# Kernel optimization log

Hardware: AMD Instinct MI355X
Metric: run time of the kernel (lower is better)

## Reference

```python
import jax, jax.numpy as jnp
import numpy as np

P, T, L, K, N, K2, M, D = 16384, 8, 4096, 16, 2048, 32, 8, 64
ITER = 8
MM = {'flow_traffic': (0.0, 1e-4), 'flow_packets': (0.0, 1e-3), 'flow_packet_size': (0.0, 1e-3), 'link_capacity': (0.0, 1e-2)}


def _mlp2(x, w1, b1, w2, b2):
    return jax.nn.relu(jax.nn.relu(x @ w1 + b1) @ w2 + b2)


def _gru(x_proj, h, wh, bh):
    # Keras GRUCell, reset_after=True, gate order (z, r, h)
    hp = h @ wh + bh
    xz, xr, xc = jnp.split(x_proj, 3, axis=-1)
    hz, hr, hc = jnp.split(hp, 3, axis=-1)
    z = jax.nn.sigmoid(xz + hz)
    r = jax.nn.sigmoid(xr + hr)
    c = jnp.tanh(xc + r * hc)
    return z * h + (1.0 - z) * c


def setup_inputs() -> dict:
    key = jax.random.key(0)
    ks = iter(jax.random.split(key, 64))
    f32, i32 = jnp.float32, jnp.int32
    rn = lambda shape: jax.random.normal(next(ks), shape, dtype=f32) * 0.05
    inp = {}
    inp['flow_traffic'] = jax.random.uniform(next(ks), (P, 1), f32, 1.0, 1000.0)
    inp['flow_packets'] = jax.random.uniform(next(ks), (P, 1), f32, 1.0, 100.0)
    inp['flow_packet_size'] = jax.random.uniform(next(ks), (P, 1), f32, 64.0, 1500.0)
    inp['link_capacity'] = jax.random.uniform(next(ks), (L, 1), f32, 10.0, 100.0)
    inp['pe_w1'] = rn((3, D)); inp['pe_b1'] = jnp.zeros((D,), f32)
    inp['pe_w2'] = rn((D, D)); inp['pe_b2'] = jnp.zeros((D,), f32)
    inp['le_w1'] = rn((3, D)); inp['le_b1'] = jnp.zeros((D,), f32)
    inp['le_w2'] = rn((D, D)); inp['le_b2'] = jnp.zeros((D,), f32)
    inp['de_w1'] = rn((2, D)); inp['de_b1'] = jnp.zeros((D,), f32)
    inp['de_w2'] = rn((D, D)); inp['de_b2'] = jnp.zeros((D,), f32)
    for p in ('pgru', 'lgru', 'dgru'):
        inp[p + '_wx'] = rn((D, 3 * D)); inp[p + '_wh'] = rn((D, 3 * D))
        inp[p + '_bx'] = jnp.zeros((3 * D,), f32); inp[p + '_bh'] = jnp.zeros((3 * D,), f32)
    inp['ro_w1'] = rn((D, D // 2)); inp['ro_b1'] = jnp.zeros((D // 2,), f32)
    inp['ro_w2'] = rn((D // 2, D // 4)); inp['ro_b2'] = jnp.zeros((D // 4,), f32)
    inp['ro_w3'] = rn((D // 4, 1)); inp['ro_b3'] = jnp.zeros((1,), f32)
    inp['link_to_path'] = jax.random.randint(next(ks), (P, T), 0, L, i32)
    inp['node_to_path'] = jax.random.randint(next(ks), (P, T), 0, N, i32)
    inp['path_to_link'] = jnp.stack([jax.random.randint(next(ks), (L, K), 0, P, i32),
                                     jax.random.randint(next(ks), (L, K), 1, T + 1, i32)], axis=-1)
    inp['path_to_node'] = jnp.stack([jax.random.randint(next(ks), (N, K2), 0, P, i32),
                                     jax.random.randint(next(ks), (N, K2), 1, T + 1, i32)], axis=-1)
    inp['link_to_node'] = jax.random.randint(next(ks), (N, M), 0, L, i32)
    inp['nodes'] = jnp.zeros((N,), i32)
    inp['link_device_type'] = jnp.zeros((L,), i32)
    return inp


def reference(flow_traffic, flow_packets, flow_packet_size, link_capacity,
              pe_w1, pe_b1, pe_w2, pe_b2, le_w1, le_b1, le_w2, le_b2,
              de_w1, de_b1, de_w2, de_b2,
              pgru_wx, pgru_wh, pgru_bx, pgru_bh,
              lgru_wx, lgru_wh, lgru_bx, lgru_bh,
              dgru_wx, dgru_wh, dgru_bx, dgru_bh,
              ro_w1, ro_b1, ro_w2, ro_b2, ro_w3, ro_b3,
              link_to_path, node_to_path, path_to_link, path_to_node,
              link_to_node, nodes, link_device_type):
    # one_hot depth=1 -> 1.0 iff value==0
    ldt = (link_device_type == 0).astype(jnp.float32)[:, None]  # [L,1]
    # link load from path traffic
    load = flow_traffic[path_to_link[:, :, 0]].sum(axis=1) / (link_capacity * 1e9)  # [L,1]
    path_in = jnp.concatenate([
        (flow_traffic - MM['flow_traffic'][0]) * MM['flow_traffic'][1],
        (flow_packets - MM['flow_packets'][0]) * MM['flow_packets'][1],
        (flow_packet_size - MM['flow_packet_size'][0]) * MM['flow_packet_size'][1]], axis=1)
    path_state = _mlp2(path_in, pe_w1, pe_b1, pe_w2, pe_b2)  # [P,D]
    link_in = jnp.concatenate([(link_capacity - MM['link_capacity'][0]) * MM['link_capacity'][1], load, ldt], axis=1)
    link_state = _mlp2(link_in, le_w1, le_b1, le_w2, le_b2)  # [L,D]
    device_link_mean = link_state[link_to_node].sum(axis=1).mean(axis=1, keepdims=True)  # [N,1]
    devices_encoded = (nodes == 0).astype(jnp.float32)[:, None]  # [N,1]
    device_state = _mlp2(jnp.concatenate([devices_encoded, device_link_mean], axis=1),
                         de_w1, de_b1, de_w2, de_b2)  # [N,D]
    pl0, pl1 = path_to_link[:, :, 0], path_to_link[:, :, 1]
    pn0, pn1 = path_to_node[:, :, 0], path_to_node[:, :, 1]
    pss = None
    for _ in range(ITER):
        x = link_state[link_to_path] + device_state[node_to_path]  # [P,T,D]
        prev = path_state
        x_proj = jnp.swapaxes(x @ pgru_wx + pgru_bx, 0, 1)  # [T,P,3D]

        def step(h, xp):
            h2 = _gru(xp, h, pgru_wh, pgru_bh)
            return h2, h2

        path_state, seq = jax.lax.scan(step, path_state, x_proj)
        pss = jnp.concatenate([prev[:, None], jnp.swapaxes(seq, 0, 1)], axis=1)  # [P,T+1,D]
        link_state = _gru(pss[pl0, pl1].sum(axis=1) @ lgru_wx + lgru_bx, link_state, lgru_wh, lgru_bh)
        device_state = _gru(pss[pn0, pn1].sum(axis=1) @ dgru_wx + dgru_bx, device_state, dgru_wh, dgru_bh)
    h = jax.nn.relu(pss[:, 1:] @ ro_w1 + ro_b1)
    h = jax.nn.relu(h @ ro_w2 + ro_b2)
    occupancy = jax.nn.softplus(h @ ro_w3 + ro_b3)  # [P,T,1]
    delay = (occupancy / link_capacity[link_to_path]).sum(axis=1)  # [P,1]
    return delay
```

## Files before the change

kernel.cpp:

```cpp
#include <hip/hip_runtime.h>
#include <hip/hip_bf16.h>

static constexpr int PN = 16384;
static constexpr int TT = 8;
static constexpr int LN = 4096;
static constexpr int KG = 16;
static constexpr int NN = 2048;
static constexpr int K2G = 32;
static constexpr int MG = 8;
static constexpr int ITER = 8;

typedef __attribute__((ext_vector_type(8))) short short8b;
typedef __attribute__((ext_vector_type(4))) float f32x4;
typedef __attribute__((ext_vector_type(4))) unsigned int u32x4;

__device__ __forceinline__ float frcp(float x) {
    return __builtin_amdgcn_rcpf(x);
}
__device__ __forceinline__ float sigmoidf_(float x) {
    return frcp(1.0f + __expf(-x));
}
__device__ __forceinline__ float tanhf_(float x) {
    return 1.0f - 2.0f * frcp(__expf(2.0f * x) + 1.0f);
}
__device__ __forceinline__ float softplusf_(float x) {
    return fmaxf(x, 0.0f) + log1pf(__expf(-fabsf(x)));
}
__device__ __forceinline__ unsigned short f2bf(float f) {
    unsigned int x = __float_as_uint(f);
    unsigned int r = (x + 0x7fffu + ((x >> 16) & 1u)) >> 16;
    return (unsigned short)r;
}
__device__ __forceinline__ unsigned int pk2bf(float a, float b) {
    union { __hip_bfloat162 h; unsigned int u; } cvt;
    cvt.h = __float22bfloat162_rn(float2{a, b});
    return cvt.u;
}
__device__ __forceinline__ float bf2f(unsigned short u) {
    return __uint_as_float(((unsigned int)u) << 16);
}

__global__ __launch_bounds__(256) void k_setup(
    const float* __restrict__ ft, const float* __restrict__ fpk,
    const float* __restrict__ fps, const float* __restrict__ cap,
    const int* __restrict__ ptl, const int* __restrict__ ldt,
    const float* __restrict__ pe_w1, const float* __restrict__ pe_b1,
    const float* __restrict__ pe_w2, const float* __restrict__ pe_b2,
    const float* __restrict__ le_w1, const float* __restrict__ le_b1,
    const float* __restrict__ le_w2, const float* __restrict__ le_b2,
    const float* __restrict__ pgru_wx, const float* __restrict__ pgru_wh,
    const float* __restrict__ lgru_wx, const float* __restrict__ lgru_wh,
    const float* __restrict__ dgru_wx, const float* __restrict__ dgru_wh,
    unsigned short* __restrict__ pwxT, unsigned short* __restrict__ pwhT,
    unsigned short* __restrict__ lwxT, unsigned short* __restrict__ lwhT,
    unsigned short* __restrict__ dwxT, unsigned short* __restrict__ dwhT,
    float* __restrict__ path_state, float* __restrict__ link_state)
{
    int b = blockIdx.x;
    int tid = threadIdx.x;
    if (b >= 1280) {
        const float* srcs[6] = {pgru_wx, pgru_wh, lgru_wx, lgru_wh, dgru_wx, dgru_wh};
        unsigned short* dsts[6] = {pwxT, pwhT, lwxT, lwhT, dwxT, dwhT};
        int i = (b - 1280) * 256 + tid;
        int mi = i / 12288, o = i - mi * 12288;
        int n = o >> 6, k = o & 63;
        dsts[mi][o] = f2bf(srcs[mi][k * 192 + n]);
        return;
    }
    __shared__ __align__(16) float w2s[4096];
    __shared__ float w1s[192], b1s[64], b2s[64];
    __shared__ float h1s[4][64];
    bool isPath = (b < 1024);
    const float* w1p = isPath ? pe_w1 : le_w1;
    const float* b1p = isPath ? pe_b1 : le_b1;
    const float* w2p = isPath ? pe_w2 : le_w2;
    const float* b2p = isPath ? pe_b2 : le_b2;
    for (int i = tid; i < 4096; i += 256) w2s[i] = w2p[i];
    if (tid < 192) w1s[tid] = w1p[tid];
    if (tid < 64) { b1s[tid] = b1p[tid]; b2s[tid] = b2p[tid]; }
    __syncthreads();
    int rl = tid >> 6, d = tid & 63;
    int base = (isPath ? b : (b - 1024)) * 16;
    for (int rp = 0; rp < 4; ++rp) {
        int row = base + rp * 4 + rl;
        float h;
        if (isPath) {
            float x0 = ft[row]  * 1e-4f;
            float x1 = fpk[row] * 1e-3f;
            float x2 = fps[row] * 1e-3f;
            h = b1s[d] + x0 * w1s[d] + x1 * w1s[64 + d] + x2 * w1s[128 + d];
        } else {
            float v = 0.0f;
            if (d < 16) v = ft[ptl[(row * 16 + d) * 2]];
            v += __shfl_down(v, 8);
            v += __shfl_down(v, 4);
            v += __shfl_down(v, 2);
            v += __shfl_down(v, 1);
            float ssum = __shfl(v, 0);
            float cv = cap[row];
            float load = ssum * frcp(cv * 1e9f);
            float x2 = (ldt[row] == 0) ? 1.0f : 0.0f;
            h = b1s[d] + cv * 0.01f * w1s[d] + load * w1s[64 + d] + x2 * w1s[128 + d];
        }
        h1s[rl][d] = fmaxf(h, 0.0f);
        __syncthreads();
        float acc = b2s[d];
#pragma unroll 8
        for (int k = 0; k < 64; ++k) acc += h1s[rl][k] * w2s[k * 64 + d];
        float* dst = isPath ? path_state : link_state;
        dst[(size_t)row * 64 + d] = fmaxf(acc, 0.0f);
        __syncthreads();
    }
}

__global__ __launch_bounds__(256) void k_device_encode(
    const float* __restrict__ link_state, const int* __restrict__ ltn,
    const int* __restrict__ nodes,
    const float* __restrict__ w1, const float* __restrict__ b1,
    const float* __restrict__ w2, const float* __restrict__ b2,
    float* __restrict__ device_state)
{
    __shared__ __align__(16) float w2s[4096];
    __shared__ float h1s[4][64];
    int tid = threadIdx.x;
    for (int i = tid; i < 4096; i += 256) w2s[i] = w2[i];
    int rl = tid >> 6, d = tid & 63;
    int row = blockIdx.x * 4 + rl;
    float s = 0.0f;
#pragma unroll
    for (int m = 0; m < MG; ++m)
        s += link_state[(size_t)ltn[row * MG + m] * 64 + d];
#pragma unroll
    for (int o = 32; o > 0; o >>= 1) s += __shfl_xor(s, o);
    float dlm = s * (1.0f / 64.0f);
    float enc = (nodes[row] == 0) ? 1.0f : 0.0f;
    float h = b1[d] + enc * w1[d] + dlm * w1[64 + d];
    h1s[rl][d] = fmaxf(h, 0.0f);
    __syncthreads();
    float acc = b2[d];
#pragma unroll 8
    for (int k = 0; k < 64; ++k) acc += h1s[rl][k] * w2s[k * 64 + d];
    device_state[(size_t)row * 64 + d] = fmaxf(acc, 0.0f);
}

template <bool LAST>
__global__ __launch_bounds__(256, 4) void k_pscan(
    const float* __restrict__ ls, const float* __restrict__ dst,
    const int* __restrict__ ltp, const int* __restrict__ ntp,
    const unsigned short* __restrict__ wxT,
    const unsigned short* __restrict__ whT,
    const float* __restrict__ bx, const float* __restrict__ bh,
    float* __restrict__ path_state, unsigned short* __restrict__ pssb,
    const float* __restrict__ rw1, const float* __restrict__ rb1,
    const float* __restrict__ rw2, const float* __restrict__ rb2,
    const float* __restrict__ rw3, const float* __restrict__ rb3,
    const float* __restrict__ cap, float* __restrict__ out)
{
    __shared__ __align__(16) unsigned short Xs[8][16][72];
    __shared__ __align__(16) unsigned short Hb0[16][72];
    __shared__ int sIdx[256];
    __shared__ __align__(16) float rw1s[LAST ? 2048 : 4];
    __shared__ __align__(16) float rw2s[LAST ? 512 : 4];
    __shared__ float rw3s[16], rb1s[32], rb2s[16];
    int tid = threadIdx.x;
    int p0 = blockIdx.x * 16;

    if (LAST) {
        for (int i = tid; i < 2048; i += 256) rw1s[i] = rw1[i];
        for (int i = tid; i < 512; i += 256) rw2s[i] = rw2[i];
        if (tid < 16) rw3s[tid] = rw3[tid];
        if (tid < 32) rb1s[tid] = rb1[tid];
        if (tid < 16) rb2s[tid] = rb2[tid];
    }
    {
        int pi = tid >> 1;
        int m = pi & 15, t = pi >> 4;
        int gi = (p0 + m) * TT + t;
        sIdx[tid] = (tid & 1) ? __builtin_nontemporal_load(ntp + gi)
                              : __builtin_nontemporal_load(ltp + gi);
    }
    __syncthreads();
    {
        int j = tid & 15;
        int g = tid >> 4;
#pragma unroll
        for (int ro = 0; ro < 8; ++ro) {
            int pi = ro * 16 + g;
            int il = sIdx[pi * 2];
            int in = sIdx[pi * 2 + 1];
            float4 a = *(const float4*)(ls + (size_t)il * 64 + j * 4);
            float4 b = *(const float4*)(dst + (size_t)in * 64 + j * 4);
            uint2 u;
            u.x = pk2bf(a.x + b.x, a.y + b.y);
            u.y = pk2bf(a.z + b.z, a.w + b.w);
            *(uint2*)&Xs[ro][g][j * 4] = u;
        }
    }

    int lane = tid & 63, w = tid >> 6;
    int c = lane & 15, q = lane >> 4;
    int d = 16 * w + c;
    short8b fx[3][2], fh[3][2];
#pragma unroll
    for (int g = 0; g < 3; ++g)
#pragma unroll
        for (int kt = 0; kt < 2; ++kt) {
            int off = (g * 64 + 16 * w + c) * 64 + kt * 32 + q * 8;
            fx[g][kt] = *(const short8b*)(wxT + off);
            fh[g][kt] = *(const short8b*)(whT + off);
        }
    float bz = bx[d] + bh[d];
    float br = bx[64 + d] + bh[64 + d];
    float bxc = bx[128 + d];
    float bhc = bh[128 + d];
    float hold[4];
#pragma unroll
    for (int r_ = 0; r_ < 4; ++r_) {
        hold[r_] = path_state[(size_t)(p0 + q * 4 + r_) * 64 + d];
        Hb0[q * 4 + r_][d] = f2bf(hold[r_]);
    }
    __syncthreads();

    short8b aXc0 = *(const short8b*)&Xs[0][c][q * 8];
    short8b aXc1 = *(const short8b*)&Xs[0][c][32 + q * 8];

    for (int t = 0; t < TT; ++t) {
        f32x4 ax[3], ah[3];
        ax[0] = (f32x4){bz, bz, bz, bz};
        ax[1] = (f32x4){br, br, br, br};
        ax[2] = (f32x4){bxc, bxc, bxc, bxc};
        ah[0] = (f32x4){0.f, 0.f, 0.f, 0.f};
        ah[1] = (f32x4){0.f, 0.f, 0.f, 0.f};
        ah[2] = (f32x4){bhc, bhc, bhc, bhc};
        const unsigned short* hsrc = (t == 0) ? &Hb0[0][0] : &Xs[t - 1][0][0];
        short8b aH0 = *(const short8b*)(hsrc + c * 72 + q * 8);
        short8b aH1 = *(const short8b*)(hsrc + c * 72 + 32 + q * 8);
#pragma unroll
        for (int g = 0; g < 3; ++g) {
            ax[g] = __builtin_amdgcn_mfma_f32_16x16x32_bf16(aXc0, fx[g][0], ax[g], 0, 0, 0);
            ax[g] = __builtin_amdgcn_mfma_f32_16x16x32_bf16(aXc1, fx[g][1], ax[g], 0, 0, 0);
            ah[g] = __builtin_amdgcn_mfma_f32_16x16x32_bf16(aH0, fh[g][0], ah[g], 0, 0, 0);
            ah[g] = __builtin_amdgcn_mfma_f32_16x16x32_bf16(aH1, fh[g][1], ah[g], 0, 0, 0);
        }
        if (t < TT - 1) {
            aXc0 = *(const short8b*)&Xs[t + 1][c][q * 8];
            aXc1 = *(const short8b*)&Xs[t + 1][c][32 + q * 8];
        }
#pragma unroll
        for (int r_ = 0; r_ < 4; ++r_) {
            float z  = sigmoidf_(ax[0][r_] + ah[0][r_]);
            float rr = sigmoidf_(ax[1][r_] + ah[1][r_]);
            float cc = tanhf_(ax[2][r_] + rr * ah[2][r_]);
            float hn = cc + z * (hold[r_] - cc);
            hold[r_] = hn;
            Xs[t][q * 4 + r_][d] = f2bf(hn);
        }
        __syncthreads();
    }
    if (!LAST) {
#pragma unroll
        for (int r_ = 0; r_ < 4; ++r_)
            path_state[(size_t)(p0 + q * 4 + r_) * 64 + d] = hold[r_];
        {
            unsigned short* base = pssb + (size_t)p0 * TT * 64;
#pragma unroll
            for (int j = 0; j < 4; ++j) {
                int o = j * 2048 + tid * 8;
                int r = o >> 6;
                int c0 = o & 63;
                int m = r >> 3, t = r & 7;
                u32x4 v = *(const u32x4*)&Xs[t][m][c0];
                __builtin_nontemporal_store(v, (u32x4*)(base + o));
            }
        }
        return;
    }
    {
        int r = tid >> 1, hh = tid & 1;
        int m = r >> 3, t = r & 7;
        short8b rowv[8];
#pragma unroll
        for (int j = 0; j < 8; ++j)
            rowv[j] = *(const short8b*)&Xs[t][m][j * 8];
        float a1[16];
#pragma unroll
        for (int i = 0; i < 16; ++i) a1[i] = 0.f;
#pragma unroll 4
        for (int k = 0; k < 64; ++k) {
            float x = bf2f((unsigned short)rowv[k >> 3][k & 7]);
            const float* wr = &rw1s[k * 32 + hh * 16];
            float4 wa = *(const float4*)(wr);
            float4 wb = *(const float4*)(wr + 4);
            float4 wc = *(const float4*)(wr + 8);
            float4 wd = *(const float4*)(wr + 12);
            a1[0]  += x * wa.x; a1[1]  += x * wa.y; a1[2]  += x * wa.z; a1[3]  += x * wa.w;
            a1[4]  += x * wb.x; a1[5]  += x * wb.y; a1[6]  += x * wb.z; a1[7]  += x * wb.w;
            a1[8]  += x * wc.x; a1[9]  += x * wc.y; a1[10] += x * wc.z; a1[11] += x * wc.w;
            a1[12] += x * wd.x; a1[13] += x * wd.y; a1[14] += x * wd.z; a1[15] += x * wd.w;
        }
#pragma unroll
        for (int i = 0; i < 16; ++i)
            a1[i] = fmaxf(a1[i] + rb1s[hh * 16 + i], 0.0f);
        float h1[32];
#pragma unroll
        for (int i = 0; i < 16; ++i) {
            float o = __shfl_xor(a1[i], 1);
            h1[hh * 16 + i] = a1[i];
            h1[(1 - hh) * 16 + i] = o;
        }
        float a2[8];
#pragma unroll
        for (int i = 0; i < 8; ++i) a2[i] = 0.f;
#pragma unroll 4
        for (int k = 0; k < 32; ++k) {
            float x = h1[k];
            const float* wr = &rw2s[k * 16 + hh * 8];
            float4 wa = *(const float4*)(wr);
            float4 wb = *(const float4*)(wr + 4);
            a2[0] += x * wa.x; a2[1] += x * wa.y; a2[2] += x * wa.z; a2[3] += x * wa.w;
            a2[4] += x * wb.x; a2[5] += x * wb.y; a2[6] += x * wb.z; a2[7] += x * wb.w;
        }
#pragma unroll
        for (int i = 0; i < 8; ++i)
            a2[i] = fmaxf(a2[i] + rb2s[hh * 8 + i], 0.0f);
        float h2[16];
#pragma unroll
        for (int i = 0; i < 8; ++i) {
            float o = __shfl_xor(a2[i], 1);
            h2[hh * 8 + i] = a2[i];
            h2[(1 - hh) * 8 + i] = o;
        }
        float a3 = rb3[0];
#pragma unroll
        for (int k = 0; k < 16; ++k) a3 += h2[k] * rw3s[k];
        float occ = softplusf_(a3);
        float dcon = occ * frcp(cap[ltp[(p0 + m) * TT + t]]);
        float s = dcon;
        s += __shfl_xor(s, 2);
        s += __shfl_xor(s, 4);
        s += __shfl_xor(s, 8);
        if ((tid & 15) == 0) out[p0 + m] = s;
    }
}

template <int Kg>
__device__ __forceinline__ void edge_body(
    const unsigned short* __restrict__ wxT, const unsigned short* __restrict__ whT,
    const float* __restrict__ bx, const float* __restrict__ bh,
    const int* __restrict__ p2e, const unsigned short* __restrict__ pssb,
    float* __restrict__ state, int blk)
{
    __shared__ int idxs[16 * Kg * 2];
    __shared__ __align__(16) unsigned short Ab[16][72];
    __shared__ __align__(16) unsigned short Hbs[16][72];
    __shared__ __align__(16) float Hf[16][68];
    int tid = threadIdx.x;
    int r0 = blk * 16;
    for (int i = tid; i < 16 * Kg * 2; i += 256)
        idxs[i] = p2e[(size_t)r0 * Kg * 2 + i];
    __syncthreads();
    {
        int r = tid >> 4, c4 = (tid & 15) * 4;
        int row = r0 + r;
        float4 s = {0.f, 0.f, 0.f, 0.f};
#pragma unroll
        for (int k = 0; k < Kg; ++k) {
            int pi = idxs[(r * Kg + k) * 2];
            int ti = idxs[(r * Kg + k) * 2 + 1];
            ushort4 v = *(const ushort4*)(pssb + ((size_t)pi * TT + ti - 1) * 64 + c4);
            s.x += bf2f(v.x); s.y += bf2f(v.y);
            s.z += bf2f(v.z); s.w += bf2f(v.w);
        }
        uint2 ua;
        ua.x = pk2bf(s.x, s.y); ua.y = pk2bf(s.z, s.w);
        *(uint2*)&Ab[r][c4] = ua;
        float4 hv = *(const float4*)(state + (size_t)row * 64 + c4);
        *(float4*)&Hf[r][c4] = hv;
        uint2 uh;
        uh.x = pk2bf(hv.x, hv.y); uh.y = pk2bf(hv.z, hv.w);
        *(uint2*)&Hbs[r][c4] = uh;
    }
    __syncthreads();
    int lane = tid & 63, w = tid >> 6;
    int c = lane & 15, q = lane >> 4;
    int d = 16 * w + c;
    short8b fx[3][2], fh[3][2];
#pragma unroll
    for (int g = 0; g < 3; ++g)
#pragma unroll
        for (int kt = 0; kt < 2; ++kt) {
            int off = (g * 64 + 16 * w + c) * 64 + kt * 32 + q * 8;
            fx[g][kt] = *(const short8b*)(wxT + off);
            fh[g][kt] = *(const short8b*)(whT + off);
        }
    float bz = bx[d] + bh[d];
    float br = bx[64 + d] + bh[64 + d];
    float bxc = bx[128 + d];
    float bhc = bh[128 + d];
    f32x4 ax[3], ah[3];
    ax[0] = (f32x4){bz, bz, bz, bz};
    ax[1] = (f32x4){br, br, br, br};
    ax[2] = (f32x4){bxc, bxc, bxc, bxc};
    ah[0] = (f32x4){0.f, 0.f, 0.f, 0.f};
    ah[1] = (f32x4){0.f, 0.f, 0.f, 0.f};
    ah[2] = (f32x4){bhc, bhc, bhc, bhc};
#pragma unroll
    for (int kt = 0; kt < 2; ++kt) {
        short8b aA = *(const short8b*)&Ab[c][kt * 32 + q * 8];
        short8b aH = *(const short8b*)&Hbs[c][kt * 32 + q * 8];
#pragma unroll
        for (int g = 0; g < 3; ++g) {
            ax[g] = __builtin_amdgcn_mfma_f32_16x16x32_bf16(aA, fx[g][kt], ax[g], 0, 0, 0);
            ah[g] = __builtin_amdgcn_mfma_f32_16x16x32_bf16(aH, fh[g][kt], ah[g], 0, 0, 0);
        }
    }
#pragma unroll
    for (int r = 0; r < 4; ++r) {
        int m = q * 4 + r;
        float z  = sigmoidf_(ax[0][r] + ah[0][r]);
        float rr = sigmoidf_(ax[1][r] + ah[1][r]);
        float cc = tanhf_(ax[2][r] + rr * ah[2][r]);
        float hn = cc + z * (Hf[m][d] - cc);
        state[(size_t)(r0 + m) * 64 + d] = hn;
    }
}

__global__ __launch_bounds__(256) void k_edge_merged(
    const unsigned short* __restrict__ lwxT, const unsigned short* __restrict__ lwhT,
    const float* __restrict__ lbx, const float* __restrict__ lbh,
    const int* __restrict__ ptl,
    const unsigned short* __restrict__ dwxT, const unsigned short* __restrict__ dwhT,
    const float* __restrict__ dbx, const float* __restrict__ dbh,
    const int* __restrict__ ptn,
    const unsigned short* __restrict__ pssb,
    float* __restrict__ link_state, float* __restrict__ device_state)
{
    int b = blockIdx.x;
    if (b < LN / 16) {
        edge_body<KG>(lwxT, lwhT, lbx, lbh, ptl, pssb, link_state, b);
    } else {
        edge_body<K2G>(dwxT, dwhT, dbx, dbh, ptn, pssb, device_state, b - LN / 16);
    }
}

extern "C" void kernel_launch(void* const* d_in, const int* in_sizes, int n_in,
                              void* d_out, int out_size, void* d_ws, size_t ws_size,
                              hipStream_t stream) {
    const float* ft   = (const float*)d_in[0];
    const float* fpk  = (const float*)d_in[1];
    const float* fps  = (const float*)d_in[2];
    const float* cap  = (const float*)d_in[3];
    const float* pe_w1 = (const float*)d_in[4];
    const float* pe_b1 = (const float*)d_in[5];
    const float* pe_w2 = (const float*)d_in[6];
    const float* pe_b2 = (const float*)d_in[7];
    const float* le_w1 = (const float*)d_in[8];
    const float* le_b1 = (const float*)d_in[9];
    const float* le_w2 = (const float*)d_in[10];
    const float* le_b2 = (const float*)d_in[11];
    const float* de_w1 = (const float*)d_in[12];
    const float* de_b1 = (const float*)d_in[13];
    const float* de_w2 = (const float*)d_in[14];
    const float* de_b2 = (const float*)d_in[15];
    const float* pgru_wx = (const float*)d_in[16];
    const float* pgru_wh = (const float*)d_in[17];
    const float* pgru_bx = (const float*)d_in[18];
    const float* pgru_bh = (const float*)d_in[19];
    const float* lgru_wx = (const float*)d_in[20];
    const float* lgru_wh = (const float*)d_in[21];
    const float* lgru_bx = (const float*)d_in[22];
    const float* lgru_bh = (const float*)d_in[23];
    const float* dgru_wx = (const float*)d_in[24];
    const float* dgru_wh = (const float*)d_in[25];
    const float* dgru_bx = (const float*)d_in[26];
    const float* dgru_bh = (const float*)d_in[27];
    const float* ro_w1 = (const float*)d_in[28];
    const float* ro_b1 = (const float*)d_in[29];
    const float* ro_w2 = (const float*)d_in[30];
    const float* ro_b2 = (const float*)d_in[31];
    const float* ro_w3 = (const float*)d_in[32];
    const float* ro_b3 = (const float*)d_in[33];
    const int* ltp   = (const int*)d_in[34];
    const int* ntp   = (const int*)d_in[35];
    const int* ptl   = (const int*)d_in[36];
    const int* ptn   = (const int*)d_in[37];
    const int* ltn   = (const int*)d_in[38];
    const int* nodes = (const int*)d_in[39];
    const int* ldt   = (const int*)d_in[40];
    float* out = (float*)d_out;

    char* ws = (char*)d_ws;
    float* path_state = (float*)ws;      ws += (size_t)PN * 64 * 4;
    float* link_state = (float*)ws;      ws += (size_t)LN * 64 * 4;
    float* device_state = (float*)ws;    ws += (size_t)NN * 64 * 4;
    unsigned short* pssb = (unsigned short*)ws; ws += (size_t)PN * TT * 64 * 2;
    unsigned short* pwxT = (unsigned short*)ws; ws += 192 * 64 * 2;
    unsigned short* pwhT = (unsigned short*)ws; ws += 192 * 64 * 2;
    unsigned short* lwxT = (unsigned short*)ws; ws += 192 * 64 * 2;
    unsigned short* lwhT = (unsigned short*)ws; ws += 192 * 64 * 2;
    unsigned short* dwxT = (unsigned short*)ws; ws += 192 * 64 * 2;
    unsigned short* dwhT = (unsigned short*)ws; ws += 192 * 64 * 2;

    k_setup<<<1568, 256, 0, stream>>>(ft, fpk, fps, cap, ptl, ldt,
                                      pe_w1, pe_b1, pe_w2, pe_b2,
                                      le_w1, le_b1, le_w2, le_b2,
                                      pgru_wx, pgru_wh, lgru_wx, lgru_wh,
                                      dgru_wx, dgru_wh,
                                      pwxT, pwhT, lwxT, lwhT, dwxT, dwhT,
                                      path_state, link_state);
    k_device_encode<<<NN / 4, 256, 0, stream>>>(link_state, ltn, nodes, de_w1,
                                                de_b1, de_w2, de_b2, device_state);
    for (int it = 0; it < ITER - 1; ++it) {
        k_pscan<false><<<PN / 16, 256, 0, stream>>>(
            link_state, device_state, ltp, ntp, pwxT, pwhT, pgru_bx, pgru_bh,
            path_state, pssb, ro_w1, ro_b1, ro_w2, ro_b2, ro_w3, ro_b3, cap, out);
        k_edge_merged<<<LN / 16 + NN / 16, 256, 0, stream>>>(
            lwxT, lwhT, lgru_bx, lgru_bh, ptl,
            dwxT, dwhT, dgru_bx, dgru_bh, ptn,
            pssb, link_state, device_state);
    }
    k_pscan<true><<<PN / 16, 256, 0, stream>>>(
        link_state, device_state, ltp, ntp, pwxT, pwhT, pgru_bx, pgru_bh,
        path_state, pssb, ro_w1, ro_b1, ro_w2, ro_b2, ro_w3, ro_b3, cap, out);
}
```

Before: 388.3 us.

## Make each wave own 16 paths in k_pscan to drop block barriers

Restructures the path GRU scan so each wavefront independently processes 16 paths across all 64 output columns, with per-wave shared-memory slices. The block grows to 64 paths and the per-timestep __syncthreads disappear, since each wave only reads its own LDS region. It removes barrier stalls in the serial 8-step recurrence. In exchange each wave holds all 48 weight fragments in registers and launch bounds drop to 1, which raises register pressure and may lower occupancy. There are also 4x fewer blocks.

```diff
diff --git a/kernel.cpp b/kernel.cpp
--- a/kernel.cpp
+++ b/kernel.cpp
@@ -144,7 +144,7 @@
 }
 
 template <bool LAST>
-__global__ __launch_bounds__(256, 4) void k_pscan(
+__global__ __launch_bounds__(256, 1) void k_pscan(
     const float* __restrict__ ls, const float* __restrict__ dst,
     const int* __restrict__ ltp, const int* __restrict__ ntp,
     const unsigned short* __restrict__ wxT,
@@ -156,14 +156,16 @@
     const float* __restrict__ rw3, const float* __restrict__ rb3,
     const float* __restrict__ cap, float* __restrict__ out)
 {
-    __shared__ __align__(16) unsigned short Xs[8][16][72];
-    __shared__ __align__(16) unsigned short Hb0[16][72];
-    __shared__ int sIdx[256];
+    __shared__ __align__(16) unsigned short Xs[4][8][16][72];
+    __shared__ __align__(16) unsigned short Hb0[4][16][72];
+    __shared__ int sIdx[4][256];
     __shared__ __align__(16) float rw1s[LAST ? 2048 : 4];
     __shared__ __align__(16) float rw2s[LAST ? 512 : 4];
     __shared__ float rw3s[16], rb1s[32], rb2s[16];
     int tid = threadIdx.x;
-    int p0 = blockIdx.x * 16;
+    int wi = tid >> 6, lane = tid & 63;
+    int c = lane & 15, q = lane >> 4;
+    int p0w = blockIdx.x * 64 + wi * 16;
 
     if (LAST) {
         for (int i = tid; i < 2048; i += 256) rw1s[i] = rw1[i];
@@ -172,174 +174,201 @@
         if (tid < 32) rb1s[tid] = rb1[tid];
         if (tid < 16) rb2s[tid] = rb2[tid];
     }
-    {
-        int pi = tid >> 1;
+
+    unsigned short (*XsW)[16][72] = Xs[wi];
+    unsigned short (*Hb0W)[72] = Hb0[wi];
+    int* sIdxW = sIdx[wi];
+
+#pragma unroll
+    for (int k = 0; k < 4; ++k) {
+        int i = k * 64 + lane;
+        int pi = i >> 1;
         int m = pi & 15, t = pi >> 4;
-        int gi = (p0 + m) * TT + t;
-        sIdx[tid] = (tid & 1) ? __builtin_nontemporal_load(ntp + gi)
-                              : __builtin_nontemporal_load(ltp + gi);
-    }
-    __syncthreads();
-    {
-        int j = tid & 15;
-        int g = tid >> 4;
-#pragma unroll
-        for (int ro = 0; ro < 8; ++ro) {
-            int pi = ro * 16 + g;
-            int il = sIdx[pi * 2];
-            int in = sIdx[pi * 2 + 1];
-            float4 a = *(const float4*)(ls + (size_t)il * 64 + j * 4);
-            float4 b = *(const float4*)(dst + (size_t)in * 64 + j * 4);
-            uint2 u;
-            u.x = pk2bf(a.x + b.x, a.y + b.y);
-            u.y = pk2bf(a.z + b.z, a.w + b.w);
-            *(uint2*)&Xs[ro][g][j * 4] = u;
-        }
-    }
-
-    int lane = tid & 63, w = tid >> 6;
-    int c = lane & 15, q = lane >> 4;
-    int d = 16 * w + c;
-    short8b fx[3][2], fh[3][2];
+        int gi = (p0w + m) * TT + t;
+        sIdxW[i] = (i & 1) ? __builtin_nontemporal_load(ntp + gi)
+                           : __builtin_nontemporal_load(ltp + gi);
+    }
+
+    short8b fx[3][4][2], fh[3][4][2];
 #pragma unroll
     for (int g = 0; g < 3; ++g)
 #pragma unroll
-        for (int kt = 0; kt < 2; ++kt) {
-            int off = (g * 64 + 16 * w + c) * 64 + kt * 32 + q * 8;
-            fx[g][kt] = *(const short8b*)(wxT + off);
-            fh[g][kt] = *(const short8b*)(whT + off);
-        }
-    float bz = bx[d] + bh[d];
-    float br = bx[64 + d] + bh[64 + d];
-    float bxc = bx[128 + d];
-    float bhc = bh[128 + d];
-    float hold[4];
-#pragma unroll
-    for (int r_ = 0; r_ < 4; ++r_) {
-        hold[r_] = path_state[(size_t)(p0 + q * 4 + r_) * 64 + d];
-        Hb0[q * 4 + r_][d] = f2bf(hold[r_]);
-    }
-    __syncthreads();
-
-    short8b aXc0 = *(const short8b*)&Xs[0][c][q * 8];
-    short8b aXc1 = *(const short8b*)&Xs[0][c][32 + q * 8];
-
+        for (int ct = 0; ct < 4; ++ct)
+#pragma unroll
+            for (int kt = 0; kt < 2; ++kt) {
+                int off = (g * 64 + ct * 16 + c) * 64 + kt * 32 + q * 8;
+                fx[g][ct][kt] = *(const short8b*)(wxT + off);
+                fh[g][ct][kt] = *(const short8b*)(whT + off);
+            }
+    float bzv[4], brv[4], bxcv[4], bhcv[4];
+#pragma unroll
+    for (int ct = 0; ct < 4; ++ct) {
+        int dd = ct * 16 + c;
+        bzv[ct]  = bx[dd] + bh[dd];
+        brv[ct]  = bx[64 + dd] + bh[64 + dd];
+        bxcv[ct] = bx[128 + dd];
+        bhcv[ct] = bh[128 + dd];
+    }
+
+#pragma unroll
+    for (int ro = 0; ro < 32; ++ro) {
+        int pi = ro * 4 + q;
+        int t = pi >> 4, m = pi & 15;
+        int il = sIdxW[pi * 2];
+        int in = sIdxW[pi * 2 + 1];
+        float4 a = *(const float4*)(ls + (size_t)il * 64 + c * 4);
+        float4 b = *(const float4*)(dst + (size_t)in * 64 + c * 4);
+        uint2 u;
+        u.x = pk2bf(a.x + b.x, a.y + b.y);
+        u.y = pk2bf(a.z + b.z, a.w + b.w);
+        *(uint2*)&XsW[t][m][c * 4] = u;
+    }
+
+    float hold[4][4];
+#pragma unroll
+    for (int r_ = 0; r_ < 4; ++r_)
+#pragma unroll
+        for (int ct = 0; ct < 4; ++ct) {
+            hold[ct][r_] = path_state[(size_t)(p0w + q * 4 + r_) * 64 + ct * 16 + c];
+            Hb0W[q * 4 + r_][ct * 16 + c] = f2bf(hold[ct][r_]);
+        }
+
+    short8b aXc0 = *(const short8b*)&XsW[0][c][q * 8];
+    short8b aXc1 = *(const short8b*)&XsW[0][c][32 + q * 8];
+#pragma unroll
     for (int t = 0; t < TT; ++t) {
-        f32x4 ax[3], ah[3];
-        ax[0] = (f32x4){bz, bz, bz, bz};
-        ax[1] = (f32x4){br, br, br, br};
-        ax[2] = (f32x4){bxc, bxc, bxc, bxc};
-        ah[0] = (f32x4){0.f, 0.f, 0.f, 0.f};
-        ah[1] = (f32x4){0.f, 0.f, 0.f, 0.f};
-        ah[2] = (f32x4){bhc, bhc, bhc, bhc};
-        const unsigned short* hsrc = (t == 0) ? &Hb0[0][0] : &Xs[t - 1][0][0];
+        const unsigned short* hsrc = (t == 0) ? &Hb0W[0][0] : &XsW[t - 1][0][0];
         short8b aH0 = *(const short8b*)(hsrc + c * 72 + q * 8);
         short8b aH1 = *(const short8b*)(hsrc + c * 72 + 32 + q * 8);
-#pragma unroll
-        for (int g = 0; g < 3; ++g) {
-            ax[g] = __builtin_amdgcn_mfma_f32_16x16x32_bf16(aXc0, fx[g][0], ax[g], 0, 0, 0);
-            ax[g] = __builtin_amdgcn_mfma_f32_16x16x32_bf16(aXc1, fx[g][1], ax[g], 0, 0, 0);
-            ah[g] = __builtin_amdgcn_mfma_f32_16x16x32_bf16(aH0, fh[g][0], ah[g], 0, 0, 0);
-            ah[g] = __builtin_amdgcn_mfma_f32_16x16x32_bf16(aH1, fh[g][1], ah[g], 0, 0, 0);
-        }
+        short8b nX0 = aXc0, nX1 = aXc1;
         if (t < TT - 1) {
-            aXc0 = *(const short8b*)&Xs[t + 1][c][q * 8];
-            aXc1 = *(const short8b*)&Xs[t + 1][c][32 + q * 8];
-        }
-#pragma unroll
-        for (int r_ = 0; r_ < 4; ++r_) {
-            float z  = sigmoidf_(ax[0][r_] + ah[0][r_]);
-            float rr = sigmoidf_(ax[1][r_] + ah[1][r_]);
-            float cc = tanhf_(ax[2][r_] + rr * ah[2][r_]);
-            float hn = cc + z * (hold[r_] - cc);
-            hold[r_] = hn;
-            Xs[t][q * 4 + r_][d] = f2bf(hn);
-        }
-        __syncthreads();
-    }
+            nX0 = *(const short8b*)&XsW[t + 1][c][q * 8];
+            nX1 = *(const short8b*)&XsW[t + 1][c][32 + q * 8];
+        }
+#pragma unroll
+        for (int ct = 0; ct < 4; ++ct) {
+            f32x4 ax0 = (f32x4){bzv[ct], bzv[ct], bzv[ct], bzv[ct]};
+            f32x4 ax1 = (f32x4){brv[ct], brv[ct], brv[ct], brv[ct]};
+            f32x4 ax2 = (f32x4){bxcv[ct], bxcv[ct], bxcv[ct], bxcv[ct]};
+            f32x4 ah0 = (f32x4){0.f, 0.f, 0.f, 0.f};
+            f32x4 ah1 = (f32x4){0.f, 0.f, 0.f, 0.f};
+            f32x4 ah2 = (f32x4){bhcv[ct], bhcv[ct], bhcv[ct], bhcv[ct]};
+            ax0 = __builtin_amdgcn_mfma_f32_16x16x32_bf16(aXc0, fx[0][ct][0], ax0, 0, 0, 0);
+            ax0 = __builtin_amdgcn_mfma_f32_16x16x32_bf16(aXc1, fx[0][ct][1], ax0, 0, 0, 0);
+            ax1 = __builtin_amdgcn_mfma_f32_16x16x32_bf16(aXc0, fx[1][ct][0], ax1, 0, 0, 0);
+            ax1 = __builtin_amdgcn_mfma_f32_16x16x32_bf16(aXc1, fx[1][ct][1], ax1, 0, 0, 0);
+            ax2 = __builtin_amdgcn_mfma_f32_16x16x32_bf16(aXc0, fx[2][ct][0], ax2, 0, 0, 0);
+            ax2 = __builtin_amdgcn_mfma_f32_16x16x32_bf16(aXc1, fx[2][ct][1], ax2, 0, 0, 0);
+            ah0 = __builtin_amdgcn_mfma_f32_16x16x32_bf16(aH0, fh[0][ct][0], ah0, 0, 0, 0);
+            ah0 = __builtin_amdgcn_mfma_f32_16x16x32_bf16(aH1, fh[0][ct][1], ah0, 0, 0, 0);
+            ah1 = __builtin_amdgcn_mfma_f32_16x16x32_bf16(aH0, fh[1][ct][0], ah1, 0, 0, 0);
+            ah1 = __builtin_amdgcn_mfma_f32_16x16x32_bf16(aH1, fh[1][ct][1], ah1, 0, 0, 0);
+            ah2 = __builtin_amdgcn_mfma_f32_16x16x32_bf16(aH0, fh[2][ct][0], ah2, 0, 0, 0);
+            ah2 = __builtin_amdgcn_mfma_f32_16x16x32_bf16(aH1, fh[2][ct][1], ah2, 0, 0, 0);
+#pragma unroll
+            for (int r_ = 0; r_ < 4; ++r_) {
+                float z  = sigmoidf_(ax0[r_] + ah0[r_]);
+                float rr = sigmoidf_(ax1[r_] + ah1[r_]);
+                float cc = tanhf_(ax2[r_] + rr * ah2[r_]);
+                float hn = cc + z * (hold[ct][r_] - cc);
+                hold[ct][r_] = hn;
+                XsW[t][q * 4 + r_][ct * 16 + c] = f2bf(hn);
+            }
+        }
+        aXc0 = nX0; aXc1 = nX1;
+    }
+
     if (!LAST) {
 #pragma unroll
         for (int r_ = 0; r_ < 4; ++r_)
-            path_state[(size_t)(p0 + q * 4 + r_) * 64 + d] = hold[r_];
+#pragma unroll
+            for (int ct = 0; ct < 4; ++ct)
+                path_state[(size_t)(p0w + q * 4 + r_) * 64 + ct * 16 + c] = hold[ct][r_];
         {
-            unsigned short* base = pssb + (size_t)p0 * TT * 64;
-#pragma unroll
-            for (int j = 0; j < 4; ++j) {
-                int o = j * 2048 + tid * 8;
+            unsigned short* base = pssb + (size_t)p0w * TT * 64;
+#pragma unroll
+            for (int jj = 0; jj < 8; ++jj) {
+                int o = jj * 512 + lane * 8;
                 int r = o >> 6;
                 int c0 = o & 63;
                 int m = r >> 3, t = r & 7;
-                u32x4 v = *(const u32x4*)&Xs[t][m][c0];
+                u32x4 v = *(const u32x4*)&XsW[t][m][c0];
                 __builtin_nontemporal_store(v, (u32x4*)(base + o));
             }
         }
         return;
     }
+    __syncthreads();
     {
-        int r = tid >> 1, hh = tid & 1;
-        int m = r >> 3, t = r & 7;
-        short8b rowv[8];
-#pragma unroll
-        for (int j = 0; j < 8; ++j)
-            rowv[j] = *(const short8b*)&Xs[t][m][j * 8];
-        float a1[16];
-#pragma unroll
-        for (int i = 0; i < 16; ++i) a1[i] = 0.f;
+        int hh = lane & 1;
+        int rl = lane >> 1;
+#pragma unroll
+        for (int pass = 0; pass < 4; ++pass) {
+            int r = pass * 32 + rl;
+            int m = r >> 3, t = r & 7;
+            short8b rowv[8];
+#pragma unroll
+            for (int j = 0; j < 8; ++j)
+                rowv[j] = *(const short8b*)&XsW[t][m][j * 8];
+            float a1[16];
+#pragma unroll
+            for (int i = 0; i < 16; ++i) a1[i] = 0.f;
 #pragma unroll 4
-        for (int k = 0; k < 64; ++k) {
-            float x = bf2f((unsigned short)rowv[k >> 3][k & 7]);
-            const float* wr = &rw1s[k * 32 + hh * 16];
-            float4 wa = *(const float4*)(wr);
-            float4 wb = *(const float4*)(wr + 4);
-            float4 wc = *(const float4*)(wr + 8);
-            float4 wd = *(const float4*)(wr + 12);
-            a1[0]  += x * wa.x; a1[1]  += x * wa.y; a1[2]  += x * wa.z; a1[3]  += x * wa.w;
-            a1[4]  += x * wb.x; a1[5]  += x * wb.y; a1[6]  += x * wb.z; a1[7]  += x * wb.w;
-            a1[8]  += x * wc.x; a1[9]  += x * wc.y; a1[10] += x * wc.z; a1[11] += x * wc.w;
-            a1[12] += x * wd.x; a1[13] += x * wd.y; a1[14] += x * wd.z; a1[15] += x * wd.w;
-        }
-#pragma unroll
-        for (int i = 0; i < 16; ++i)
-            a1[i] = fmaxf(a1[i] + rb1s[hh * 16 + i], 0.0f);
-        float h1[32];
-#pragma unroll
-        for (int i = 0; i < 16; ++i) {
-            float o = __shfl_xor(a1[i], 1);
-            h1[hh * 16 + i] = a1[i];
-            h1[(1 - hh) * 16 + i] = o;
-        }
-        float a2[8];
-#pragma unroll
-        for (int i = 0; i < 8; ++i) a2[i] = 0.f;
+            for (int k = 0; k < 64; ++k) {
+                float x = bf2f((unsigned short)rowv[k >> 3][k & 7]);
+                const float* wr = &rw1s[k * 32 + hh * 16];
+                float4 wa = *(const float4*)(wr);
+                float4 wb = *(const float4*)(wr + 4);
+                float4 wc = *(const float4*)(wr + 8);
+                float4 wd = *(const float4*)(wr + 12);
+                a1[0]  += x * wa.x; a1[1]  += x * wa.y; a1[2]  += x * wa.z; a1[3]  += x * wa.w;
+                a1[4]  += x * wb.x; a1[5]  += x * wb.y; a1[6]  += x * wb.z; a1[7]  += x * wb.w;
+                a1[8]  += x * wc.x; a1[9]  += x * wc.y; a1[10] += x * wc.z; a1[11] += x * wc.w;
+                a1[12] += x * wd.x; a1[13] += x * wd.y; a1[14] += x * wd.z; a1[15] += x * wd.w;
+            }
+#pragma unroll
+            for (int i = 0; i < 16; ++i)
+                a1[i] = fmaxf(a1[i] + rb1s[hh * 16 + i], 0.0f);
+            float h1[32];
+#pragma unroll
+            for (int i = 0; i < 16; ++i) {
+                float o = __shfl_xor(a1[i], 1);
+                h1[hh * 16 + i] = a1[i];
+                h1[(1 - hh) * 16 + i] = o;
+            }
+            float a2[8];
+#pragma unroll
+            for (int i = 0; i < 8; ++i) a2[i] = 0.f;
 #pragma unroll 4
-        for (int k = 0; k < 32; ++k) {
-            float x = h1[k];
-            const float* wr = &rw2s[k * 16 + hh * 8];
-            float4 wa = *(const float4*)(wr);
-            float4 wb = *(const float4*)(wr + 4);
-            a2[0] += x * wa.x; a2[1] += x * wa.y; a2[2] += x * wa.z; a2[3] += x * wa.w;
-            a2[4] += x * wb.x; a2[5] += x * wb.y; a2[6] += x * wb.z; a2[7] += x * wb.w;
-        }
-#pragma unroll
-        for (int i = 0; i < 8; ++i)
-            a2[i] = fmaxf(a2[i] + rb2s[hh * 8 + i], 0.0f);
-        float h2[16];
-#pragma unroll
-        for (int i = 0; i < 8; ++i) {
-            float o = __shfl_xor(a2[i], 1);
-            h2[hh * 8 + i] = a2[i];
-            h2[(1 - hh) * 8 + i] = o;
-        }
-        float a3 = rb3[0];
-#pragma unroll
-        for (int k = 0; k < 16; ++k) a3 += h2[k] * rw3s[k];
-        float occ = softplusf_(a3);
-        float dcon = occ * frcp(cap[ltp[(p0 + m) * TT + t]]);
-        float s = dcon;
-        s += __shfl_xor(s, 2);
-        s += __shfl_xor(s, 4);
-        s += __shfl_xor(s, 8);
-        if ((tid & 15) == 0) out[p0 + m] = s;
+            for (int k = 0; k < 32; ++k) {
+                float x = h1[k];
+                const float* wr = &rw2s[k * 16 + hh * 8];
+                float4 wa = *(const float4*)(wr);
+                float4 wb = *(const float4*)(wr + 4);
+                a2[0] += x * wa.x; a2[1] += x * wa.y; a2[2] += x * wa.z; a2[3] += x * wa.w;
+                a2[4] += x * wb.x; a2[5] += x * wb.y; a2[6] += x * wb.z; a2[7] += x * wb.w;
+            }
+#pragma unroll
+            for (int i = 0; i < 8; ++i)
+                a2[i] = fmaxf(a2[i] + rb2s[hh * 8 + i], 0.0f);
+            float h2[16];
+#pragma unroll
+            for (int i = 0; i < 8; ++i) {
+                float o = __shfl_xor(a2[i], 1);
+                h2[hh * 8 + i] = a2[i];
+                h2[(1 - hh) * 8 + i] = o;
+            }
+            float a3 = rb3[0];
+#pragma unroll
+            for (int k = 0; k < 16; ++k) a3 += h2[k] * rw3s[k];
+            float occ = softplusf_(a3);
+            float dcon = occ * frcp(cap[sIdxW[(t * 16 + m) * 2]]);
+            float s = dcon;
+            s += __shfl_xor(s, 2);
+            s += __shfl_xor(s, 4);
+            s += __shfl_xor(s, 8);
+            if ((lane & 15) == 0) out[p0w + pass * 4 + (lane >> 4)] = s;
+        }
     }
 }
 
@@ -511,7 +540,7 @@
     k_device_encode<<<NN / 4, 256, 0, stream>>>(link_state, ltn, nodes, de_w1,
                                                 de_b1, de_w2, de_b2, device_state);
     for (int it = 0; it < ITER - 1; ++it) {
-        k_pscan<false><<<PN / 16, 256, 0, stream>>>(
+        k_pscan<false><<<PN / 64, 256, 0, stream>>>(
             link_state, device_state, ltp, ntp, pwxT, pwhT, pgru_bx, pgru_bh,
             path_state, pssb, ro_w1, ro_b1, ro_w2, ro_b2, ro_w3, ro_b3, cap, out);
         k_edge_merged<<<LN / 16 + NN / 16, 256, 0, stream>>>(
@@ -519,7 +548,7 @@
             dwxT, dwhT, dgru_bx, dgru_bh, ptn,
             pssb, link_state, device_state);
     }
-    k_pscan<true><<<PN / 16, 256, 0, stream>>>(
+    k_pscan<true><<<PN / 64, 256, 0, stream>>>(
         link_state, device_state, ltp, ntp, pwxT, pwhT, pgru_bx, pgru_bh,
         path_state, pssb, ro_w1, ro_b1, ro_w2, ro_b2, ro_w3, ro_b3, cap, out);
 }
```

After: 675.1 us. 73.8% more time.
